# Kernel optimization log

Measured on AMD Instinct MI355X. Metric: run time of the kernel, lower is better.

## Reference

```python
import jax, jax.numpy as jnp
import numpy as np

B, H, W, D, C = 2, 16, 16, 16, 128
UNITS = 128
BN_EPS = 1e-3  # keras BatchNormalization default epsilon


def setup_inputs() -> dict:
    key = jax.random.key(0)
    ks = jax.random.split(key, 12)
    lim = np.sqrt(3.0 / C)  # VarianceScaling(1.0, fan_avg, uniform)
    inp = {
        "x": jax.random.normal(ks[0], (B, H, W, D, C), dtype=jnp.float32),
        "gamma": jnp.ones((C,), jnp.float32),
        "beta": jnp.zeros((C,), jnp.float32),
        "moving_mean": jax.random.normal(ks[1], (C,), jnp.float32) * 0.1,
        "moving_var": jnp.ones((C,), jnp.float32) + 0.1 * jax.random.uniform(ks[2], (C,)),
        "Wq": jax.random.uniform(ks[3], (C, UNITS), jnp.float32, -lim, lim),
        "bq": jnp.zeros((UNITS,), jnp.float32),
        "Wk": jax.random.uniform(ks[4], (C, UNITS), jnp.float32, -lim, lim),
        "bk": jnp.zeros((UNITS,), jnp.float32),
        "Wv": jax.random.uniform(ks[5], (C, UNITS), jnp.float32, -lim, lim),
        "bv": jnp.zeros((UNITS,), jnp.float32),
        # proj uses kernel_init(0.0) -> effectively ~0; use tiny scale to keep grads nonzero
        "Wp": jax.random.uniform(ks[6], (UNITS, UNITS), jnp.float32, -1e-5, 1e-5),
        "bp": jnp.zeros((UNITS,), jnp.float32),
    }
    return inp


def reference(x, gamma, beta, moving_mean, moving_var, Wq, bq, Wk, bk, Wv, bv, Wp, bp):
    # BatchNormalization (inference mode): per-channel affine normalization
    xn = (x - moving_mean) * jax.lax.rsqrt(moving_var + BN_EPS) * gamma + beta
    b, h, w, d, c = xn.shape
    n = h * w * d
    scale = jnp.asarray(UNITS, jnp.float32) ** -0.5
    q = (xn @ Wq + bq).reshape(b, n, UNITS)
    k = (xn @ Wk + bk).reshape(b, n, UNITS)
    v = (xn @ Wv + bv).reshape(b, n, UNITS)
    # full self-attention over flattened 3D spatial dims: [b, n, n] scores
    attn = jax.nn.softmax(jnp.einsum('bnc,bmc->bnm', q, k) * scale, axis=-1)
    proj = jnp.einsum('bnm,bmc->bnc', attn, v).reshape(b, h, w, d, UNITS)
    proj = proj @ Wp + bp
    return xn + proj
```

## Files before the change

### kernel.cpp

```cpp
#include <hip/hip_runtime.h>
#include <hip/hip_bf16.h>

using bh8     = __attribute__((ext_vector_type(8))) short;
using floatx4 = __attribute__((ext_vector_type(4))) float;
using uintx2  = __attribute__((ext_vector_type(2))) unsigned;

#define MFMA16 __builtin_amdgcn_mfma_f32_16x16x32_bf16

__device__ __forceinline__ float b2f(short s) {
    union { unsigned u; float f; } v; v.u = ((unsigned)(unsigned short)s) << 16; return v.f;
}
__device__ __forceinline__ short f2b(float f) {
    union { float f; unsigned u; } v; v.f = f;
    unsigned r = (v.u + 0x7fffu + ((v.u >> 16) & 1u)) >> 16;
    return (short)r;
}
__device__ __forceinline__ unsigned pk2(float a, float b) {
    union { __hip_bfloat162 h; unsigned u; } v;
    v.h = __float22bfloat162_rn(make_float2(a, b));
    return v.u;
}
__device__ __forceinline__ float ldf(const void* p, int i, bool f32) {
    return f32 ? ((const float*)p)[i] : b2f(((const short*)p)[i]);
}
__device__ __forceinline__ bool detect_f32(const void* gamma) {
    return ((*(const unsigned*)gamma) & 0xFFFFu) == 0u;
}
__device__ __forceinline__ void gl2lds16(const short* g, short* l) {
    __builtin_amdgcn_global_load_lds(
        (const __attribute__((address_space(1))) void*)g,
        (__attribute__((address_space(3))) void*)l, 16, 0, 0);
}

#define WAITV(N) do { asm volatile("s_waitcnt vmcnt(" #N ")" ::: "memory"); \
                      __builtin_amdgcn_sched_barrier(0); } while (0)

#define LDW 136

__global__ __launch_bounds__(256) void k_bn_qkv(
    const void* __restrict__ xp,
    const void* __restrict__ gp, const void* __restrict__ bep,
    const void* __restrict__ mmp, const void* __restrict__ mvp,
    const void* __restrict__ Wqp, const void* __restrict__ bqp,
    const void* __restrict__ Wkp, const void* __restrict__ bkp,
    const void* __restrict__ Wvp, const void* __restrict__ bvp,
    short* __restrict__ Qo, short* __restrict__ Ko, short* __restrict__ Vt)
{
    __shared__ float sS[128], sT[128];
    __shared__ __align__(16) short Wt[128 * LDW];
    const bool f32 = detect_f32(gp);
    const int tid = threadIdx.x, wave = tid >> 6, lane = tid & 63;
    const int lq = lane >> 4, lr = lane & 15;
    const int g = blockIdx.x >> 6;
    const int tile = blockIdx.x & 63;
    const int row0 = tile * 128 + wave * 32;

    if (tid < 128) {
        float ga = ldf(gp, tid, f32), be = ldf(bep, tid, f32);
        float mm = ldf(mmp, tid, f32), mv = ldf(mvp, tid, f32);
        float s = ga * rsqrtf(mv + 1e-3f);
        sS[tid] = s;
        sT[tid] = be - mm * s;
    }

    const void* W  = (g == 0) ? Wqp : ((g == 1) ? Wkp : Wvp);
    const void* bb = (g == 0) ? bqp : ((g == 1) ? bkp : bvp);

    if (f32) {
        for (int it = 0; it < 16; ++it) {
            int f = (it * 256 + tid) * 4;
            int c = f >> 7, u = f & 127;
            floatx4 wv = *(const floatx4*)((const float*)W + f);
            #pragma unroll
            for (int jj = 0; jj < 4; ++jj) {
                int j = (jj + (tid >> 1)) & 3;
                Wt[(u + j) * LDW + c] = f2b(wv[j]);
            }
        }
    } else {
        for (int it = 0; it < 8; ++it) {
            int f = (it * 256 + tid) * 8;
            int c = f >> 7, u = f & 127;
            bh8 wv = *(const bh8*)((const short*)W + f);
            #pragma unroll
            for (int jj = 0; jj < 8; ++jj) {
                int j = (jj + tid) & 7;
                Wt[(u + j) * LDW + c] = wv[j];
            }
        }
    }
    __syncthreads();

    bh8 a[2][4];
    #pragma unroll
    for (int rt = 0; rt < 2; ++rt)
        #pragma unroll
        for (int ks = 0; ks < 4; ++ks) {
            int c0 = ks * 32 + lq * 8;
            floatx4 s0 = *(const floatx4*)(&sS[c0]), s1 = *(const floatx4*)(&sS[c0 + 4]);
            floatx4 t0 = *(const floatx4*)(&sT[c0]), t1 = *(const floatx4*)(&sT[c0 + 4]);
            bh8 af;
            if (f32) {
                const float* xr = (const float*)xp + (size_t)(row0 + rt * 16 + lr) * 128 + c0;
                floatx4 x0 = *(const floatx4*)xr, x1 = *(const floatx4*)(xr + 4);
                #pragma unroll
                for (int j = 0; j < 4; ++j) {
                    af[j]     = f2b(x0[j] * s0[j] + t0[j]);
                    af[j + 4] = f2b(x1[j] * s1[j] + t1[j]);
                }
            } else {
                bh8 xv = *(const bh8*)((const short*)xp + (size_t)(row0 + rt * 16 + lr) * 128 + c0);
                #pragma unroll
                for (int j = 0; j < 4; ++j) {
                    af[j]     = f2b(b2f(xv[j]) * s0[j] + t0[j]);
                    af[j + 4] = f2b(b2f(xv[j + 4]) * s1[j] + t1[j]);
                }
            }
            a[rt][ks] = af;
        }

    floatx4 acc[2][8] = {};
    #pragma unroll
    for (int ks = 0; ks < 4; ++ks)
        #pragma unroll
        for (int t = 0; t < 8; ++t) {
            bh8 b = *(const bh8*)(&Wt[(t * 16 + lr) * LDW + ks * 32 + lq * 8]);
            #pragma unroll
            for (int rt = 0; rt < 2; ++rt)
                acc[rt][t] = MFMA16(a[rt][ks], b, acc[rt][t], 0, 0, 0);
        }

    if (g < 2) {
        #pragma unroll
        for (int t = 0; t < 8; ++t) {
            int u = t * 16 + lr;
            float bias = ldf(bb, u, f32);
            #pragma unroll
            for (int rt = 0; rt < 2; ++rt)
                #pragma unroll
                for (int r = 0; r < 4; ++r) {
                    int grow = row0 + rt * 16 + lq * 4 + r;
                    short vb = f2b(acc[rt][t][r] + bias);
                    if (g == 0) Qo[(size_t)grow * 128 + u] = vb;
                    else        Ko[(size_t)grow * 128 + u] = vb;
                }
        }
    } else {
        __syncthreads();
        short* sVt = Wt;
        #pragma unroll
        for (int t = 0; t < 8; ++t) {
            int u = t * 16 + lr;
            float bias = ldf(bb, u, f32);
            #pragma unroll
            for (int rt = 0; rt < 2; ++rt)
                #pragma unroll
                for (int r = 0; r < 4; ++r) {
                    int n = wave * 32 + rt * 16 + lq * 4 + r;
                    sVt[u * LDW + n] = f2b(acc[rt][t][r] + bias);
                }
        }
        __syncthreads();
        int u = tid >> 1, nh = tid & 1;
        int grow0 = tile * 128 + nh * 64;
        int bsb = grow0 >> 12, nn = grow0 & 4095;
        short* dst = Vt + (size_t)bsb * 128 * 4096 + (size_t)u * 4096 + nn;
        #pragma unroll
        for (int j = 0; j < 8; ++j)
            *(bh8*)(dst + j * 8) = *(const bh8*)(&sVt[u * LDW + nh * 64 + j * 8]);
    }
}

__global__ __launch_bounds__(256, 3) void k_attn(
    const short* __restrict__ Qg, const short* __restrict__ Kg,
    const short* __restrict__ Vtg, short* __restrict__ Op,
    float* __restrict__ Lq)
{
    __shared__ __align__(16) short sK[2][32 * 128];
    __shared__ __align__(16) short sV[2][128 * 32];

    const int tid = threadIdx.x, wave = tid >> 6, lane = tid & 63;
    const int lq = lane >> 4, lr = lane & 15;
    const int qt = blockIdx.x >> 3, kq = blockIdx.x & 7;
    const int mq = qt * 128, bs = mq >> 12, key0q = kq * 512;
    const short* Kb = Kg + (size_t)bs * 4096 * 128;
    const short* Vb = Vtg + (size_t)bs * 128 * 4096;
    const int qrow0 = mq + wave * 32;
    const bool lqodd = (lq & 1);

    bh8 aq[2][4];
    #pragma unroll
    for (int rt = 0; rt < 2; ++rt)
        #pragma unroll
        for (int ks = 0; ks < 4; ++ks)
            aq[rt][ks] = *(const bh8*)(Qg + (size_t)(qrow0 + rt * 16 + lr) * 128 + ks * 32 + lq * 8);

    const int kKey = lane >> 4, kCh = lane & 15;
    const int vU   = lane >> 2, vCh = lane & 3;

    floatx4 accO[2][8] = {};
    float lsum[2] = {};
    const float c2 = 0.12751743f;
    const float m2 = 11.541560f;

    auto stage = [&](int tt, int bb) {
        const int key1 = key0q + tt * 32;
        #pragma unroll
        for (int rd = 0; rd < 2; ++rd) {
            int key = wave * 8 + rd * 4 + kKey;
            gl2lds16(Kb + (size_t)(key1 + key) * 128 + ((kCh ^ (key & 7)) << 3),
                     &sK[bb][(wave * 8 + rd * 4) * 128]);
        }
        #pragma unroll
        for (int rd = 0; rd < 2; ++rd) {
            int u = wave * 32 + rd * 16 + vU;
            gl2lds16(Vb + (size_t)u * 4096 + key1 + ((vCh ^ ((u >> 1) & 3)) << 3),
                     &sV[bb][(wave * 32 + rd * 16) * 32]);
        }
    };

    auto do_tile = [&](int bb) {
        __builtin_amdgcn_s_barrier();
        __builtin_amdgcn_sched_barrier(0);
        const short* sKp = &sK[bb][0];
        const short* sVp = &sV[bb][0];

        floatx4 s[2][2];
        #pragma unroll
        for (int rt = 0; rt < 2; ++rt)
            #pragma unroll
            for (int t = 0; t < 2; ++t)
                s[rt][t] = floatx4{};
        __builtin_amdgcn_s_setprio(1);
        #pragma unroll
        for (int t = 0; t < 2; ++t)
            #pragma unroll
            for (int ks = 0; ks < 4; ++ks) {
                bh8 kf = *(const bh8*)(&sKp[(t * 16 + lr) * 128 +
                                            (((ks * 4 + lq) ^ (lr & 7)) << 3)]);
                #pragma unroll
                for (int rt = 0; rt < 2; ++rt)
                    s[rt][t] = MFMA16(kf, aq[rt][ks], s[rt][t], 0, 0, 0);
            }
        __builtin_amdgcn_s_setprio(0);

        bh8 ap[2];
        #pragma unroll
        for (int rt = 0; rt < 2; ++rt) {
            unsigned w[4];
            #pragma unroll
            for (int t = 0; t < 2; ++t) {
                float e[4];
                #pragma unroll
                for (int r = 0; r < 4; ++r) {
                    e[r] = exp2f(fmaf(s[rt][t][r], c2, -m2));
                    lsum[rt] += e[r];
                }
                w[t * 2]     = pk2(e[0], e[1]);
                w[t * 2 + 1] = pk2(e[2], e[3]);
            }
            unsigned A = w[0], B = w[1], C = w[2], D = w[3];
            asm volatile("v_permlane32_swap_b32 %0, %1" : "+v"(A), "+v"(C));
            asm volatile("v_permlane32_swap_b32 %0, %1" : "+v"(B), "+v"(D));
            unsigned E = __shfl_xor(A, 16, 64);
            unsigned F = __shfl_xor(B, 16, 64);
            unsigned G = __shfl_xor(C, 16, 64);
            unsigned H = __shfl_xor(D, 16, 64);
            union { unsigned u[4]; bh8 v; } P;
            P.u[0] = lqodd ? G : A;
            P.u[1] = lqodd ? H : B;
            P.u[2] = lqodd ? C : E;
            P.u[3] = lqodd ? D : F;
            ap[rt] = P.v;
        }

        __builtin_amdgcn_s_setprio(1);
        #pragma unroll
        for (int t = 0; t < 8; ++t) {
            int u = t * 16 + lr;
            bh8 b = *(const bh8*)(&sVp[u * 32 + ((lq ^ ((lr >> 1) & 3)) << 3)]);
            #pragma unroll
            for (int rt = 0; rt < 2; ++rt)
                accO[rt][t] = MFMA16(ap[rt], b, accO[rt][t], 0, 0, 0);
        }
        __builtin_amdgcn_s_setprio(0);
        __builtin_amdgcn_sched_barrier(0);
        __builtin_amdgcn_s_barrier();
    };

    stage(0, 0); stage(1, 1);

    #pragma unroll 2
    for (int t = 0; t < 14; ++t) {
        WAITV(4);
        do_tile(t & 1);
        stage(t + 2, t & 1);
    }
    WAITV(4); do_tile(0);
    WAITV(0); do_tile(1);

    #pragma unroll
    for (int rt = 0; rt < 2; ++rt) {
        float v = lsum[rt];
        v += __shfl_xor(v, 16, 64);
        v += __shfl_xor(v, 32, 64);
        if (lane < 16)
            Lq[(size_t)kq * 8192 + qrow0 + rt * 16 + lr] = v;
    }
    short* Ob = Op + (size_t)kq * 8192 * 128;
    #pragma unroll
    for (int rt = 0; rt < 2; ++rt)
        #pragma unroll
        for (int t = 0; t < 8; ++t)
            #pragma unroll
            for (int r = 0; r < 4; ++r)
                Ob[(size_t)(qrow0 + rt * 16 + lq * 4 + r) * 128 + t * 16 + lr]
                    = f2b(accO[rt][t][r]);
}

__global__ __launch_bounds__(256, 2) void k_proj(
    const short* __restrict__ Op, const float* __restrict__ Lq,
    const void* __restrict__ Wpp, const void* __restrict__ bpp,
    const void* __restrict__ xp,
    const void* __restrict__ gp, const void* __restrict__ bep,
    const void* __restrict__ mmp, const void* __restrict__ mvp,
    void* __restrict__ outp)
{
    __shared__ float sS[128], sT[128];
    __shared__ __align__(16) short Wt[128 * LDW];
    __shared__ __align__(16) short sO[16 * LDW];
    const bool f32 = detect_f32(gp);
    const int tid = threadIdx.x, wave = tid >> 6, lane = tid & 63;
    const int lq = lane >> 4, lr = lane & 15;
    const int row0 = blockIdx.x * 16;

    if (tid < 128) {
        float ga = ldf(gp, tid, f32), be = ldf(bep, tid, f32);
        float mm = ldf(mmp, tid, f32), mv = ldf(mvp, tid, f32);
        float s = ga * rsqrtf(mv + 1e-3f);
        sS[tid] = s;
        sT[tid] = be - mm * s;
    }

    if (f32) {
        for (int it = 0; it < 16; ++it) {
            int f = (it * 256 + tid) * 4;
            int c = f >> 7, u = f & 127;
            floatx4 wv = *(const floatx4*)((const float*)Wpp + f);
            #pragma unroll
            for (int jj = 0; jj < 4; ++jj) {
                int j = (jj + (tid >> 1)) & 3;
                Wt[(u + j) * LDW + c] = f2b(wv[j]);
            }
        }
    } else {
        for (int it = 0; it < 8; ++it) {
            int f = (it * 256 + tid) * 8;
            int c = f >> 7, u = f & 127;
            bh8 wv = *(const bh8*)((const short*)Wpp + f);
            #pragma unroll
            for (int jj = 0; jj < 8; ++jj) {
                int j = (jj + tid) & 7;
                Wt[(u + j) * LDW + c] = wv[j];
            }
        }
    }

    {
        int f = tid * 8;
        int row = f >> 7, c = f & 127;
        int grow = row0 + row;
        float L = 0.f;
        #pragma unroll
        for (int w = 0; w < 8; ++w) L += Lq[(size_t)w * 8192 + grow];
        float invL = 1.0f / L;
        float sum[8] = {};
        #pragma unroll
        for (int w = 0; w < 8; ++w) {
            bh8 p = *(const bh8*)(Op + (size_t)w * 8192 * 128 + (size_t)grow * 128 + c);
            #pragma unroll
            for (int j = 0; j < 8; ++j) sum[j] += b2f(p[j]);
        }
        bh8 o;
        #pragma unroll
        for (int j = 0; j < 8; ++j) o[j] = f2b(sum[j] * invL);
        *(bh8*)(&sO[row * LDW + c]) = o;
    }
    __syncthreads();

    bh8 a[4];
    #pragma unroll
    for (int ks = 0; ks < 4; ++ks)
        a[ks] = *(const bh8*)(&sO[lr * LDW + ks * 32 + lq * 8]);

    floatx4 acc[2] = {};
    #pragma unroll
    for (int ks = 0; ks < 4; ++ks)
        #pragma unroll
        for (int tt = 0; tt < 2; ++tt) {
            bh8 b = *(const bh8*)(&Wt[(wave * 32 + tt * 16 + lr) * LDW + ks * 32 + lq * 8]);
            acc[tt] = MFMA16(a[ks], b, acc[tt], 0, 0, 0);
        }

    #pragma unroll
    for (int tt = 0; tt < 2; ++tt) {
        int u = wave * 32 + tt * 16 + lr;
        float bias = ldf(bpp, u, f32);
        float su = sS[u], tu = sT[u];
        #pragma unroll
        for (int r = 0; r < 4; ++r) {
            int grow = row0 + lq * 4 + r;
            float xnv = ldf(xp, grow * 128 + u, f32) * su + tu;
            float v = acc[tt][r] + bias + xnv;
            size_t idx = (size_t)grow * 128 + u;
            if (f32) ((float*)outp)[idx] = v;
            else     ((short*)outp)[idx] = f2b(v);
        }
    }
}

extern "C" void kernel_launch(void* const* d_in, const int* in_sizes, int n_in,
                              void* d_out, int out_size, void* d_ws, size_t ws_size,
                              hipStream_t stream)
{
    const void* x     = d_in[0];
    const void* gamma = d_in[1];
    const void* beta  = d_in[2];
    const void* mmean = d_in[3];
    const void* mvar  = d_in[4];
    const void* Wq    = d_in[5];
    const void* bq    = d_in[6];
    const void* Wk    = d_in[7];
    const void* bk    = d_in[8];
    const void* Wv    = d_in[9];
    const void* bv    = d_in[10];
    const void* Wp    = d_in[11];
    const void* bp    = d_in[12];

    char* ws = (char*)d_ws;
    const size_t MB = 1024u * 1024u;
    short* Q     = (short*)(ws + 0 * MB);
    short* K     = (short*)(ws + 2 * MB);
    short* Vt    = (short*)(ws + 4 * MB);
    short* Opart = (short*)(ws + 6 * MB);
    float* Lsum  = (float*)(ws + 22 * MB);

    k_bn_qkv<<<192, 256, 0, stream>>>(x, gamma, beta, mmean, mvar,
                                      Wq, bq, Wk, bk, Wv, bv, Q, K, Vt);
    k_attn<<<512, 256, 0, stream>>>(Q, K, Vt, Opart, Lsum);
    k_proj<<<512, 256, 0, stream>>>(Opart, Lsum, Wp, bp, x,
                                    gamma, beta, mmean, mvar, d_out);
}
```

Measured before the change: 129.6 us.

## Load K/V fragments directly from global memory instead of LDS double-buffering

Removes the LDS double-buffered staging of K and V tiles (global_load_lds, barriers, swizzled reads) in the attention kernel. Each wave now loads its K and V MFMA fragments straight from global memory into registers every iteration, and occupancy hint drops from 3 to 2 blocks per CU. This removes barriers and LDS traffic but makes each wave fetch K/V itself with no cross-wave sharing, so L2/global traffic rises and latency is no longer hidden by explicit prefetch.

```diff
diff --git a/kernel.cpp b/kernel.cpp
--- a/kernel.cpp
+++ b/kernel.cpp
@@ -26,14 +26,6 @@
 __device__ __forceinline__ bool detect_f32(const void* gamma) {
     return ((*(const unsigned*)gamma) & 0xFFFFu) == 0u;
 }
-__device__ __forceinline__ void gl2lds16(const short* g, short* l) {
-    __builtin_amdgcn_global_load_lds(
-        (const __attribute__((address_space(1))) void*)g,
-        (__attribute__((address_space(3))) void*)l, 16, 0, 0);
-}
-
-#define WAITV(N) do { asm volatile("s_waitcnt vmcnt(" #N ")" ::: "memory"); \
-                      __builtin_amdgcn_sched_barrier(0); } while (0)
 
 #define LDW 136
 
@@ -171,14 +163,11 @@
     }
 }
 
-__global__ __launch_bounds__(256, 3) void k_attn(
+__global__ __launch_bounds__(256, 2) void k_attn(
     const short* __restrict__ Qg, const short* __restrict__ Kg,
     const short* __restrict__ Vtg, short* __restrict__ Op,
     float* __restrict__ Lq)
 {
-    __shared__ __align__(16) short sK[2][32 * 128];
-    __shared__ __align__(16) short sV[2][128 * 32];
-
     const int tid = threadIdx.x, wave = tid >> 6, lane = tid & 63;
     const int lq = lane >> 4, lr = lane & 15;
     const int qt = blockIdx.x >> 3, kq = blockIdx.x & 7;
@@ -195,69 +184,55 @@
         for (int ks = 0; ks < 4; ++ks)
             aq[rt][ks] = *(const bh8*)(Qg + (size_t)(qrow0 + rt * 16 + lr) * 128 + ks * 32 + lq * 8);
 
-    const int kKey = lane >> 4, kCh = lane & 15;
-    const int vU   = lane >> 2, vCh = lane & 3;
-
     floatx4 accO[2][8] = {};
     float lsum[2] = {};
     const float c2 = 0.12751743f;
     const float m2 = 11.541560f;
 
-    auto stage = [&](int tt, int bb) {
-        const int key1 = key0q + tt * 32;
-        #pragma unroll
-        for (int rd = 0; rd < 2; ++rd) {
-            int key = wave * 8 + rd * 4 + kKey;
-            gl2lds16(Kb + (size_t)(key1 + key) * 128 + ((kCh ^ (key & 7)) << 3),
-                     &sK[bb][(wave * 8 + rd * 4) * 128]);
-        }
-        #pragma unroll
-        for (int rd = 0; rd < 2; ++rd) {
-            int u = wave * 32 + rd * 16 + vU;
-            gl2lds16(Vb + (size_t)u * 4096 + key1 + ((vCh ^ ((u >> 1) & 3)) << 3),
-                     &sV[bb][(wave * 32 + rd * 16) * 32]);
-        }
-    };
-
-    auto do_tile = [&](int bb) {
-        __builtin_amdgcn_s_barrier();
-        __builtin_amdgcn_sched_barrier(0);
-        const short* sKp = &sK[bb][0];
-        const short* sVp = &sV[bb][0];
+    #pragma unroll 2
+    for (int t = 0; t < 16; ++t) {
+        const short* Kt = Kb + (size_t)(key0q + t * 32) * 128;
+        const short* Vt = Vb + key0q + t * 32;
+
+        bh8 kf[2][4];
+        #pragma unroll
+        for (int t2 = 0; t2 < 2; ++t2)
+            #pragma unroll
+            for (int ks = 0; ks < 4; ++ks)
+                kf[t2][ks] = *(const bh8*)(Kt + (size_t)(t2 * 16 + lr) * 128 + ks * 32 + lq * 8);
+        bh8 vf[8];
+        #pragma unroll
+        for (int t8 = 0; t8 < 8; ++t8)
+            vf[t8] = *(const bh8*)(Vt + (size_t)(t8 * 16 + lr) * 4096 + lq * 8);
 
         floatx4 s[2][2];
         #pragma unroll
         for (int rt = 0; rt < 2; ++rt)
             #pragma unroll
-            for (int t = 0; t < 2; ++t)
-                s[rt][t] = floatx4{};
-        __builtin_amdgcn_s_setprio(1);
-        #pragma unroll
-        for (int t = 0; t < 2; ++t)
-            #pragma unroll
-            for (int ks = 0; ks < 4; ++ks) {
-                bh8 kf = *(const bh8*)(&sKp[(t * 16 + lr) * 128 +
-                                            (((ks * 4 + lq) ^ (lr & 7)) << 3)]);
+            for (int t2 = 0; t2 < 2; ++t2)
+                s[rt][t2] = floatx4{};
+        #pragma unroll
+        for (int t2 = 0; t2 < 2; ++t2)
+            #pragma unroll
+            for (int ks = 0; ks < 4; ++ks)
                 #pragma unroll
                 for (int rt = 0; rt < 2; ++rt)
-                    s[rt][t] = MFMA16(kf, aq[rt][ks], s[rt][t], 0, 0, 0);
-            }
-        __builtin_amdgcn_s_setprio(0);
+                    s[rt][t2] = MFMA16(kf[t2][ks], aq[rt][ks], s[rt][t2], 0, 0, 0);
 
         bh8 ap[2];
         #pragma unroll
         for (int rt = 0; rt < 2; ++rt) {
             unsigned w[4];
             #pragma unroll
-            for (int t = 0; t < 2; ++t) {
+            for (int t2 = 0; t2 < 2; ++t2) {
                 float e[4];
                 #pragma unroll
                 for (int r = 0; r < 4; ++r) {
-                    e[r] = exp2f(fmaf(s[rt][t][r], c2, -m2));
+                    e[r] = exp2f(fmaf(s[rt][t2][r], c2, -m2));
                     lsum[rt] += e[r];
                 }
-                w[t * 2]     = pk2(e[0], e[1]);
-                w[t * 2 + 1] = pk2(e[2], e[3]);
+                w[t2 * 2]     = pk2(e[0], e[1]);
+                w[t2 * 2 + 1] = pk2(e[2], e[3]);
             }
             unsigned A = w[0], B = w[1], C = w[2], D = w[3];
             asm volatile("v_permlane32_swap_b32 %0, %1" : "+v"(A), "+v"(C));
@@ -274,30 +249,12 @@
             ap[rt] = P.v;
         }
 
-        __builtin_amdgcn_s_setprio(1);
-        #pragma unroll
-        for (int t = 0; t < 8; ++t) {
-            int u = t * 16 + lr;
-            bh8 b = *(const bh8*)(&sVp[u * 32 + ((lq ^ ((lr >> 1) & 3)) << 3)]);
+        #pragma unroll
+        for (int t8 = 0; t8 < 8; ++t8)
             #pragma unroll
             for (int rt = 0; rt < 2; ++rt)
-                accO[rt][t] = MFMA16(ap[rt], b, accO[rt][t], 0, 0, 0);
-        }
-        __builtin_amdgcn_s_setprio(0);
-        __builtin_amdgcn_sched_barrier(0);
-        __builtin_amdgcn_s_barrier();
-    };
-
-    stage(0, 0); stage(1, 1);
-
-    #pragma unroll 2
-    for (int t = 0; t < 14; ++t) {
-        WAITV(4);
-        do_tile(t & 1);
-        stage(t + 2, t & 1);
-    }
-    WAITV(4); do_tile(0);
-    WAITV(0); do_tile(1);
+                accO[rt][t8] = MFMA16(ap[rt], vf[t8], accO[rt][t8], 0, 0, 0);
+    }
 
     #pragma unroll
     for (int rt = 0; rt < 2; ++rt) {
```

Result: slower. 163.5 us (+26.1%).

## Triple-buffer K/V LDS tiles in attention kernel with one barrier per step

Applied to the files above, without the earlier changes.

Grows the K and V shared-memory staging from two buffers to three. Each step now issues the next tile's global-to-LDS load before computing the current tile, and only one barrier per step remains instead of two. The aim is to overlap loads with MFMA work and cut synchronisation stalls. In exchange, LDS use per block rises from 32 KB to 48 KB, which may reduce occupancy under launch_bounds(256,3), and the loop is now fully unrolled by hand.

```diff
diff --git a/kernel.cpp b/kernel.cpp
--- a/kernel.cpp
+++ b/kernel.cpp
@@ -176,8 +176,8 @@
     const short* __restrict__ Vtg, short* __restrict__ Op,
     float* __restrict__ Lq)
 {
-    __shared__ __align__(16) short sK[2][32 * 128];
-    __shared__ __align__(16) short sV[2][128 * 32];
+    __shared__ __align__(16) short sK[3][32 * 128];
+    __shared__ __align__(16) short sV[3][128 * 32];
 
     const int tid = threadIdx.x, wave = tid >> 6, lane = tid & 63;
     const int lq = lane >> 4, lr = lane & 15;
@@ -220,8 +220,6 @@
     };
 
     auto do_tile = [&](int bb) {
-        __builtin_amdgcn_s_barrier();
-        __builtin_amdgcn_sched_barrier(0);
         const short* sKp = &sK[bb][0];
         const short* sVp = &sV[bb][0];
 
@@ -229,18 +227,18 @@
         #pragma unroll
         for (int rt = 0; rt < 2; ++rt)
             #pragma unroll
-            for (int t = 0; t < 2; ++t)
-                s[rt][t] = floatx4{};
+            for (int t2 = 0; t2 < 2; ++t2)
+                s[rt][t2] = floatx4{};
         __builtin_amdgcn_s_setprio(1);
         #pragma unroll
-        for (int t = 0; t < 2; ++t)
+        for (int t2 = 0; t2 < 2; ++t2)
             #pragma unroll
             for (int ks = 0; ks < 4; ++ks) {
-                bh8 kf = *(const bh8*)(&sKp[(t * 16 + lr) * 128 +
+                bh8 kf = *(const bh8*)(&sKp[(t2 * 16 + lr) * 128 +
                                             (((ks * 4 + lq) ^ (lr & 7)) << 3)]);
                 #pragma unroll
                 for (int rt = 0; rt < 2; ++rt)
-                    s[rt][t] = MFMA16(kf, aq[rt][ks], s[rt][t], 0, 0, 0);
+                    s[rt][t2] = MFMA16(kf, aq[rt][ks], s[rt][t2], 0, 0, 0);
             }
         __builtin_amdgcn_s_setprio(0);
 
@@ -249,15 +247,15 @@
         for (int rt = 0; rt < 2; ++rt) {
             unsigned w[4];
             #pragma unroll
-            for (int t = 0; t < 2; ++t) {
+            for (int t2 = 0; t2 < 2; ++t2) {
                 float e[4];
                 #pragma unroll
                 for (int r = 0; r < 4; ++r) {
-                    e[r] = exp2f(fmaf(s[rt][t][r], c2, -m2));
+                    e[r] = exp2f(fmaf(s[rt][t2][r], c2, -m2));
                     lsum[rt] += e[r];
                 }
-                w[t * 2]     = pk2(e[0], e[1]);
-                w[t * 2 + 1] = pk2(e[2], e[3]);
+                w[t2 * 2]     = pk2(e[0], e[1]);
+                w[t2 * 2 + 1] = pk2(e[2], e[3]);
             }
             unsigned A = w[0], B = w[1], C = w[2], D = w[3];
             asm volatile("v_permlane32_swap_b32 %0, %1" : "+v"(A), "+v"(C));
@@ -276,28 +274,36 @@
 
         __builtin_amdgcn_s_setprio(1);
         #pragma unroll
-        for (int t = 0; t < 8; ++t) {
-            int u = t * 16 + lr;
+        for (int t8 = 0; t8 < 8; ++t8) {
+            int u = t8 * 16 + lr;
             bh8 b = *(const bh8*)(&sVp[u * 32 + ((lq ^ ((lr >> 1) & 3)) << 3)]);
             #pragma unroll
             for (int rt = 0; rt < 2; ++rt)
-                accO[rt][t] = MFMA16(ap[rt], b, accO[rt][t], 0, 0, 0);
+                accO[rt][t8] = MFMA16(ap[rt], b, accO[rt][t8], 0, 0, 0);
         }
         __builtin_amdgcn_s_setprio(0);
-        __builtin_amdgcn_sched_barrier(0);
-        __builtin_amdgcn_s_barrier();
     };
 
+    #define STEP(T, BB, BS) do {                         \
+        WAITV(4);                                        \
+        __builtin_amdgcn_s_barrier();                    \
+        __builtin_amdgcn_sched_barrier(0);               \
+        stage((T) + 2, (BS));                            \
+        do_tile((BB));                                   \
+    } while (0)
+
     stage(0, 0); stage(1, 1);
 
-    #pragma unroll 2
-    for (int t = 0; t < 14; ++t) {
-        WAITV(4);
-        do_tile(t & 1);
-        stage(t + 2, t & 1);
-    }
-    WAITV(4); do_tile(0);
-    WAITV(0); do_tile(1);
+    STEP(0, 0, 2);  STEP(1, 1, 0);  STEP(2, 2, 1);
+    STEP(3, 0, 2);  STEP(4, 1, 0);  STEP(5, 2, 1);
+    STEP(6, 0, 2);  STEP(7, 1, 0);  STEP(8, 2, 1);
+    STEP(9, 0, 2);  STEP(10, 1, 0); STEP(11, 2, 1);
+    STEP(12, 0, 2); STEP(13, 1, 0);
+    WAITV(4); __builtin_amdgcn_s_barrier(); __builtin_amdgcn_sched_barrier(0);
+    do_tile(2);
+    WAITV(0); __builtin_amdgcn_s_barrier(); __builtin_amdgcn_sched_barrier(0);
+    do_tile(0);
+    #undef STEP
 
     #pragma unroll
     for (int rt = 0; rt < 2; ++rt) {
```

New measurement: 154.8 us. 19.4% more time.
